# Performance work log

Measured on AMD Instinct MI355X. Metric: run time of the kernel, lower is better.

The kernel has to match this reference:

```python
import jax, jax.numpy as jnp
import numpy as np

E = 8        # num_experts
K = 2        # experts_per_token
D = 1024     # embed_dim
F = 4096     # expert intermediate (mlp_ratio * D)
FS = 2048    # shared-expert intermediate (n_shared_experts * D)
B, S = 2, 1024


def setup_inputs() -> dict:
    key = jax.random.key(0)
    ks = jax.random.split(key, 8)
    scale = jnp.float32(0.02)
    return {
        "x": jax.random.normal(ks[0], (B, S, D), jnp.float32),
        "gate_w": jax.random.normal(ks[1], (E, D), jnp.float32) * scale,
        "gate_k": jax.random.normal(ks[2], (E, D, F), jnp.float32) * scale,
        "up_k": jax.random.normal(ks[3], (E, D, F), jnp.float32) * scale,
        "down_k": jax.random.normal(ks[4], (E, F, D), jnp.float32) * scale,
        "sh_gate": jax.random.normal(ks[5], (D, FS), jnp.float32) * scale,
        "sh_up": jax.random.normal(ks[6], (D, FS), jnp.float32) * scale,
        "sh_down": jax.random.normal(ks[7], (FS, D), jnp.float32) * scale,
    }


def reference(x, gate_w, gate_k, up_k, down_k, sh_gate, sh_up, sh_down):
    b, s, d = x.shape
    xt = x.reshape(-1, d)                                   # [N, D] tokens

    # --- router gate: softmax over expert logits, then top-k ---
    logits = xt @ gate_w.T                                  # [N, E]
    scores = jax.nn.softmax(logits, axis=-1)
    topk_w, topk_i = jax.lax.top_k(scores, K)               # [N, K] each
    # norm_topk_prob = False -> use raw softmax top-k weights

    # per-token combine weights over experts: [N, E]
    combine = (jax.nn.one_hot(topk_i, E, dtype=xt.dtype) * topk_w[..., None]).sum(axis=1)

    # --- routed experts: SwiGLU MLP per expert (batched over E) ---
    g = jnp.einsum("nd,edf->enf", xt, gate_k)               # [E, N, F]
    u = jnp.einsum("nd,edf->enf", xt, up_k)                 # [E, N, F]
    a = jax.nn.silu(g) * u                                  # [E, N, F]
    eo = jnp.einsum("enf,efd->end", a, down_k)              # [E, N, D]
    y = jnp.einsum("end,ne->nd", eo, combine)               # [N, D]

    # --- shared expert (SwiGLU) on identity input ---
    shared = (jax.nn.silu(xt @ sh_gate) * (xt @ sh_up)) @ sh_down  # [N, D]

    return (y + shared).reshape(b, s, d)
```

## Files before the change

kernel.cpp:

```cpp
#include <hip/hip_runtime.h>
#include <hip/hip_bf16.h>

#define E_ 8
#define K_ 2
#define D_ 1024
#define F_ 4096
#define FS_ 2048
#define N_ 2048
#define ROWS_CAP 4352
#define TILE_CAP 40

typedef __bf16 bf16x8 __attribute__((ext_vector_type(8)));
typedef float f32x4 __attribute__((ext_vector_type(4)));

static __device__ __forceinline__ unsigned short f2bf(float f) {
  union { float f; unsigned int u; } v; v.f = f;
  unsigned int u = v.u;
  return (unsigned short)((u + 0x7FFF + ((u >> 16) & 1)) >> 16);
}

static __device__ __forceinline__ void gload16(const unsigned short* gp, unsigned short* lp) {
  __builtin_amdgcn_global_load_lds(
      (const __attribute__((address_space(1))) unsigned int*)gp,
      (__attribute__((address_space(3))) unsigned int*)lp, 16, 0, 0);
}

__global__ void init_k(int* counts) {
  if (threadIdx.x < E_) counts[threadIdx.x] = 0;
}

__global__ void router_k(const float* __restrict__ x, const float* __restrict__ gw,
                         unsigned short* __restrict__ xbf, float* __restrict__ topw,
                         int* __restrict__ topi, int* __restrict__ counts) {
  int wave = threadIdx.x >> 6, lane = threadIdx.x & 63;
  int n = blockIdx.x * 4 + wave;
  const float* xr = x + (size_t)n * D_;
  float v[16];
#pragma unroll
  for (int j = 0; j < 16; ++j) v[j] = xr[lane + 64 * j];
#pragma unroll
  for (int j = 0; j < 16; ++j) xbf[(size_t)n * D_ + lane + 64 * j] = f2bf(v[j]);
  float logit[E_];
  for (int e = 0; e < E_; ++e) {
    const float* g = gw + e * D_;
    float acc = 0.f;
#pragma unroll
    for (int j = 0; j < 16; ++j) acc += v[j] * g[lane + 64 * j];
#pragma unroll
    for (int off = 32; off > 0; off >>= 1) acc += __shfl_down(acc, off, 64);
    logit[e] = __shfl(acc, 0, 64);
  }
  if (lane == 0) {
    float m = logit[0];
    for (int e = 1; e < E_; ++e) m = fmaxf(m, logit[e]);
    float p[E_], s = 0.f;
    for (int e = 0; e < E_; ++e) { p[e] = expf(logit[e] - m); s += p[e]; }
    float inv = 1.f / s;
    for (int e = 0; e < E_; ++e) p[e] *= inv;
    int i0 = 0;
    for (int e = 1; e < E_; ++e) if (p[e] > p[i0]) i0 = e;
    int i1 = (i0 == 0) ? 1 : 0;
    for (int e = 0; e < E_; ++e) if (e != i0 && p[e] > p[i1]) i1 = e;
    topi[n * 2] = i0; topi[n * 2 + 1] = i1;
    topw[n * 2] = p[i0]; topw[n * 2 + 1] = p[i1];
    atomicAdd(&counts[i0], 1);
    atomicAdd(&counts[i1], 1);
  }
}

__global__ void scan_k(const int* __restrict__ counts, int* __restrict__ offs,
                       int* __restrict__ cursor, int* __restrict__ tile_e,
                       int* __restrict__ tile_m, int* __restrict__ ntiles) {
  if (threadIdx.x == 0) {
    int o = 0, idx = 0;
    for (int e = 0; e < E_; ++e) {
      offs[e] = o;
      int c = counts[e];
      int mt = (c + 127) >> 7;
      for (int m = 0; m < mt; ++m) {
        if (idx < TILE_CAP) { tile_e[idx] = e; tile_m[idx] = m; ++idx; }
      }
      o += c; cursor[e] = 0;
    }
    offs[E_] = o;
    ntiles[0] = idx;
  }
}

__global__ void fill_k(const int* __restrict__ topi, const int* __restrict__ offs,
                       int* __restrict__ cursor, int* __restrict__ rowlist,
                       int* __restrict__ slot_of) {
  int n = blockIdx.x * blockDim.x + threadIdx.x;
  if (n >= N_) return;
  for (int k = 0; k < K_; ++k) {
    int e = topi[n * 2 + k];
    int pos = offs[e] + atomicAdd(&cursor[e], 1);
    rowlist[pos] = n;
    slot_of[n * 2 + k] = pos;
  }
}

__global__ void transpose_cvt_k(const float* __restrict__ in, unsigned short* __restrict__ out,
                                int R, int C) {
  __shared__ float tile[64][65];
  int cb = blockIdx.x * 64, rb = blockIdx.y * 64;
  const float* ip = in + (size_t)blockIdx.z * R * C;
  unsigned short* op = out + (size_t)blockIdx.z * R * C;
  int t = threadIdx.x;
  int cx = t & 63, ry = t >> 6;
#pragma unroll
  for (int i = 0; i < 16; ++i)
    tile[ry + i * 4][cx] = ip[(size_t)(rb + ry + i * 4) * C + cb + cx];
  __syncthreads();
  int wx = t & 31, wy = t >> 5;
#pragma unroll
  for (int i = 0; i < 8; ++i) {
    int cl = wy + i * 8;
    unsigned int u = (unsigned int)f2bf(tile[2 * wx][cl]) |
                     ((unsigned int)f2bf(tile[2 * wx + 1][cl]) << 16);
    ((unsigned int*)(op + (size_t)(cb + cl) * R + rb))[wx] = u;
  }
}

__launch_bounds__(256, 3)
__global__ void gemm1_k(const unsigned short* __restrict__ Abase,
                        const int* __restrict__ rowlist,
                        const int* __restrict__ offs,
                        const int* __restrict__ tile_e, const int* __restrict__ tile_m,
                        const int* __restrict__ ntiles, int Mfixed,
                        const unsigned short* __restrict__ Bg_base,
                        const unsigned short* __restrict__ Bu_base,
                        int Ncols, int Kdim,
                        unsigned short* __restrict__ Out) {
  int e, mbase, Me, slotbase;
  if (tile_e) {
    if ((int)blockIdx.x >= ntiles[0]) return;
    e = tile_e[blockIdx.x]; mbase = tile_m[blockIdx.x] * 128;
    slotbase = offs[e]; Me = offs[e + 1] - slotbase;
  } else {
    e = 0; mbase = blockIdx.x * 128; slotbase = 0; Me = Mfixed;
  }
  int nbase = blockIdx.y * 64;
  const unsigned short* Bg = Bg_base + (size_t)e * Ncols * Kdim;
  const unsigned short* Bu = Bu_base + (size_t)e * Ncols * Kdim;

  __shared__ unsigned short As[128 * 32];
  __shared__ unsigned short Bgs[64 * 32];
  __shared__ unsigned short Bus[64 * 32];

  int t = threadIdx.x, lane = t & 63, wave = t >> 6;
  int wm = wave >> 1, wn = wave & 1;
  int chunk = lane & 3, rsub = lane >> 2;

  const unsigned short* aptr[2];
  unsigned int aoff[2];
#pragma unroll
  for (int i = 0; i < 2; ++i) {
    int r = wave * 32 + i * 16 + rsub;
    int grow = mbase + r;
    int src;
    if (rowlist) src = rowlist[slotbase + ((grow < Me) ? grow : 0)];
    else src = (grow < Me) ? grow : 0;
    aptr[i] = Abase + (size_t)src * Kdim + chunk * 8;
    aoff[i] = (unsigned)(wave * 32 + i * 16) * 32;
  }
  int bn = nbase + wave * 16 + rsub;
  const unsigned short* bgptr = Bg + (size_t)bn * Kdim + chunk * 8;
  const unsigned short* buptr = Bu + (size_t)bn * Kdim + chunk * 8;
  unsigned int boff = (unsigned)(wave * 16) * 32;

  f32x4 accg[4][2], accu[4][2];
#pragma unroll
  for (int i = 0; i < 4; ++i)
#pragma unroll
    for (int j = 0; j < 2; ++j) {
      accg[i][j] = f32x4{0.f, 0.f, 0.f, 0.f};
      accu[i][j] = f32x4{0.f, 0.f, 0.f, 0.f};
    }

  int nk = Kdim >> 5;
  for (int kt = 0; kt < nk; ++kt) {
    gload16(aptr[0] + kt * 32, &As[aoff[0]]);
    gload16(aptr[1] + kt * 32, &As[aoff[1]]);
    gload16(bgptr + kt * 32, &Bgs[boff]);
    gload16(buptr + kt * 32, &Bus[boff]);
    __syncthreads();
    bf16x8 afr[4];
#pragma unroll
    for (int i = 0; i < 4; ++i)
      afr[i] = *(const bf16x8*)&As[(wm * 64 + i * 16 + (lane & 15)) * 32 + (lane >> 4) * 8];
#pragma unroll
    for (int j = 0; j < 2; ++j) {
      bf16x8 bg = *(const bf16x8*)&Bgs[(wn * 32 + j * 16 + (lane & 15)) * 32 + (lane >> 4) * 8];
      bf16x8 bu = *(const bf16x8*)&Bus[(wn * 32 + j * 16 + (lane & 15)) * 32 + (lane >> 4) * 8];
#pragma unroll
      for (int i = 0; i < 4; ++i) {
        accg[i][j] = __builtin_amdgcn_mfma_f32_16x16x32_bf16(afr[i], bg, accg[i][j], 0, 0, 0);
        accu[i][j] = __builtin_amdgcn_mfma_f32_16x16x32_bf16(afr[i], bu, accu[i][j], 0, 0, 0);
      }
    }
    __syncthreads();
  }
  int r0 = (lane >> 4) * 4, cn = lane & 15;
#pragma unroll
  for (int i = 0; i < 4; ++i) {
#pragma unroll
    for (int rr = 0; rr < 4; ++rr) {
      int grow = mbase + wm * 64 + i * 16 + r0 + rr;
      if (grow < Me) {
        size_t rbase = (size_t)(slotbase + grow) * Ncols + nbase;
#pragma unroll
        for (int j = 0; j < 2; ++j) {
          float g = accg[i][j][rr], u = accu[i][j][rr];
          float a = (g / (1.f + __expf(-g))) * u;
          Out[rbase + wn * 32 + j * 16 + cn] = f2bf(a);
        }
      }
    }
  }
}

__launch_bounds__(256, 3)
__global__ void gemm2_k(const unsigned short* __restrict__ Abase,
                        const int* __restrict__ offs,
                        const int* __restrict__ tile_e, const int* __restrict__ tile_m,
                        const int* __restrict__ ntiles, int Mfixed,
                        const unsigned short* __restrict__ Bt_base,
                        int Ncols, int Kdim, int kchunk,
                        float* __restrict__ Out) {
  int e, mbase, Me, slotbase;
  if (tile_e) {
    if ((int)blockIdx.x >= ntiles[0]) return;
    e = tile_e[blockIdx.x]; mbase = tile_m[blockIdx.x] * 128;
    slotbase = offs[e]; Me = offs[e + 1] - slotbase;
  } else {
    e = 0; mbase = blockIdx.x * 128; slotbase = 0; Me = Mfixed;
  }
  int nbase = blockIdx.y * 128;
  int koff = blockIdx.z * kchunk;
  const unsigned short* Bt = Bt_base + (size_t)e * Ncols * Kdim;

  __shared__ unsigned short As[128 * 32];
  __shared__ unsigned short Bs[128 * 32];

  int t = threadIdx.x, lane = t & 63, wave = t >> 6;
  int wm = wave >> 1, wn = wave & 1;
  int chunk = lane & 3, rsub = lane >> 2;

  const unsigned short* aptr[2];
  const unsigned short* bptr[2];
  unsigned int loff[2];
#pragma unroll
  for (int i = 0; i < 2; ++i) {
    int r = wave * 32 + i * 16 + rsub;
    int grow = mbase + r;
    int arow = slotbase + ((grow < Me) ? grow : 0);
    aptr[i] = Abase + (size_t)arow * Kdim + koff + chunk * 8;
    bptr[i] = Bt + (size_t)(nbase + r) * Kdim + koff + chunk * 8;
    loff[i] = (unsigned)(wave * 32 + i * 16) * 32;
  }

  f32x4 acc[4][4];
#pragma unroll
  for (int i = 0; i < 4; ++i)
#pragma unroll
    for (int j = 0; j < 4; ++j) acc[i][j] = f32x4{0.f, 0.f, 0.f, 0.f};

  int nk = kchunk >> 5;
  for (int kt = 0; kt < nk; ++kt) {
    gload16(aptr[0] + kt * 32, &As[loff[0]]);
    gload16(aptr[1] + kt * 32, &As[loff[1]]);
    gload16(bptr[0] + kt * 32, &Bs[loff[0]]);
    gload16(bptr[1] + kt * 32, &Bs[loff[1]]);
    __syncthreads();
    bf16x8 afr[4];
#pragma unroll
    for (int i = 0; i < 4; ++i)
      afr[i] = *(const bf16x8*)&As[(wm * 64 + i * 16 + (lane & 15)) * 32 + (lane >> 4) * 8];
#pragma unroll
    for (int j = 0; j < 4; ++j) {
      bf16x8 bb = *(const bf16x8*)&Bs[(wn * 64 + j * 16 + (lane & 15)) * 32 + (lane >> 4) * 8];
#pragma unroll
      for (int i = 0; i < 4; ++i)
        acc[i][j] = __builtin_amdgcn_mfma_f32_16x16x32_bf16(afr[i], bb, acc[i][j], 0, 0, 0);
    }
    __syncthreads();
  }
  int r0 = (lane >> 4) * 4, cn = lane & 15;
#pragma unroll
  for (int i = 0; i < 4; ++i) {
#pragma unroll
    for (int rr = 0; rr < 4; ++rr) {
      int grow = mbase + wm * 64 + i * 16 + r0 + rr;
      if (grow < Me) {
        size_t rbase = (size_t)(slotbase + grow) * Ncols + nbase;
#pragma unroll
        for (int j = 0; j < 4; ++j)
          atomicAdd(&Out[rbase + wn * 64 + j * 16 + cn], acc[i][j][rr]);
      }
    }
  }
}

__launch_bounds__(256, 2)
__global__ void gemm1_old(const unsigned short* __restrict__ Abase,
                          const int* __restrict__ rowlist,
                          const int* __restrict__ offs, int Mfixed,
                          const float* __restrict__ Bg_base,
                          const float* __restrict__ Bu_base,
                          int Ncols, int Kdim,
                          unsigned short* __restrict__ Out) {
  int e = blockIdx.z;
  int Me, slotbase;
  if (offs) { slotbase = offs[e]; Me = offs[e + 1] - slotbase; }
  else      { slotbase = 0;       Me = Mfixed; }
  int mbase = blockIdx.x * 128;
  if (mbase >= Me) return;
  int nbase = blockIdx.y * 128;
  const float* Bg = Bg_base + (size_t)e * Kdim * Ncols;
  const float* Bu = Bu_base + (size_t)e * Kdim * Ncols;
  __shared__ unsigned short As[128][40];
  __shared__ unsigned short Bgs[128][40];
  __shared__ unsigned short Bus[128][40];
  int t = threadIdx.x, lane = t & 63, wave = t >> 6;
  int wm = wave >> 1, wn = wave & 1;
  f32x4 accg[4][4], accu[4][4];
#pragma unroll
  for (int i = 0; i < 4; ++i)
#pragma unroll
    for (int j = 0; j < 4; ++j) {
      accg[i][j] = f32x4{0.f, 0.f, 0.f, 0.f};
      accu[i][j] = f32x4{0.f, 0.f, 0.f, 0.f};
    }
  int ar = t >> 1, akh = t & 1;
  int arow = mbase + ar;
  int asrc = 0;
  if (arow < Me) asrc = rowlist ? rowlist[slotbase + arow] : arow;
  const unsigned short* aptr = Abase + (size_t)asrc * Kdim + akh * 16;
  int bfc = t & 127, bkh = t >> 7;
  const float* bgp = Bg + (size_t)(bkh * 16) * Ncols + nbase + bfc;
  const float* bup = Bu + (size_t)(bkh * 16) * Ncols + nbase + bfc;
  int nk = Kdim >> 5;
  for (int kt = 0; kt < nk; ++kt) {
    uint4 a0 = *(const uint4*)(aptr + kt * 32);
    uint4 a1 = *(const uint4*)(aptr + kt * 32 + 8);
    *(uint4*)&As[ar][akh * 16] = a0;
    *(uint4*)&As[ar][akh * 16 + 8] = a1;
    {
      const float* p0 = bgp + (size_t)kt * 32 * Ncols;
      float bv[16]; unsigned short h[16];
#pragma unroll
      for (int i = 0; i < 16; ++i) bv[i] = p0[(size_t)i * Ncols];
#pragma unroll
      for (int i = 0; i < 16; ++i) h[i] = f2bf(bv[i]);
      *(uint4*)&Bgs[bfc][bkh * 16] = *(uint4*)&h[0];
      *(uint4*)&Bgs[bfc][bkh * 16 + 8] = *(uint4*)&h[8];
    }
    {
      const float* p1 = bup + (size_t)kt * 32 * Ncols;
      float bv[16]; unsigned short h[16];
#pragma unroll
      for (int i = 0; i < 16; ++i) bv[i] = p1[(size_t)i * Ncols];
#pragma unroll
      for (int i = 0; i < 16; ++i) h[i] = f2bf(bv[i]);
      *(uint4*)&Bus[bfc][bkh * 16] = *(uint4*)&h[0];
      *(uint4*)&Bus[bfc][bkh * 16 + 8] = *(uint4*)&h[8];
    }
    __syncthreads();
    bf16x8 afr[4];
#pragma unroll
    for (int i = 0; i < 4; ++i)
      afr[i] = *(const bf16x8*)&As[wm * 64 + i * 16 + (lane & 15)][(lane >> 4) * 8];
#pragma unroll
    for (int j = 0; j < 4; ++j) {
      bf16x8 bg = *(const bf16x8*)&Bgs[wn * 64 + j * 16 + (lane & 15)][(lane >> 4) * 8];
      bf16x8 bu = *(const bf16x8*)&Bus[wn * 64 + j * 16 + (lane & 15)][(lane >> 4) * 8];
#pragma unroll
      for (int i = 0; i < 4; ++i) {
        accg[i][j] = __builtin_amdgcn_mfma_f32_16x16x32_bf16(afr[i], bg, accg[i][j], 0, 0, 0);
        accu[i][j] = __builtin_amdgcn_mfma_f32_16x16x32_bf16(afr[i], bu, accu[i][j], 0, 0, 0);
      }
    }
    __syncthreads();
  }
  int r0 = (lane >> 4) * 4, cn = lane & 15;
#pragma unroll
  for (int i = 0; i < 4; ++i) {
#pragma unroll
    for (int rr = 0; rr < 4; ++rr) {
      int grow = mbase + wm * 64 + i * 16 + r0 + rr;
      if (grow < Me) {
        size_t rbase = (size_t)(slotbase + grow) * Ncols + nbase;
#pragma unroll
        for (int j = 0; j < 4; ++j) {
          float g = accg[i][j][rr], u = accu[i][j][rr];
          float a = (g / (1.f + __expf(-g))) * u;
          Out[rbase + wn * 64 + j * 16 + cn] = f2bf(a);
        }
      }
    }
  }
}

__launch_bounds__(256, 2)
__global__ void gemm2_old(const unsigned short* __restrict__ Abase,
                          const int* __restrict__ offs, int Mfixed,
                          const float* __restrict__ B_base,
                          int Ncols, int Kdim,
                          float* __restrict__ Out) {
  int e = blockIdx.z;
  int Me, slotbase;
  if (offs) { slotbase = offs[e]; Me = offs[e + 1] - slotbase; }
  else      { slotbase = 0;       Me = Mfixed; }
  int mbase = blockIdx.x * 128;
  if (mbase >= Me) return;
  int nbase = blockIdx.y * 128;
  const float* B = B_base + (size_t)e * Kdim * Ncols;
  __shared__ unsigned short As[128][40];
  __shared__ unsigned short Bs[128][40];
  int t = threadIdx.x, lane = t & 63, wave = t >> 6;
  int wm = wave >> 1, wn = wave & 1;
  f32x4 acc[4][4];
#pragma unroll
  for (int i = 0; i < 4; ++i)
#pragma unroll
    for (int j = 0; j < 4; ++j) acc[i][j] = f32x4{0.f, 0.f, 0.f, 0.f};
  int ar = t >> 1, akh = t & 1;
  int arow = slotbase + ((mbase + ar < Me) ? (mbase + ar) : 0);
  const unsigned short* aptr = Abase + (size_t)arow * Kdim + akh * 16;
  int bfc = t & 127, bkh = t >> 7;
  const float* bp = B + (size_t)(bkh * 16) * Ncols + nbase + bfc;
  int nk = Kdim >> 5;
  for (int kt = 0; kt < nk; ++kt) {
    uint4 a0 = *(const uint4*)(aptr + kt * 32);
    uint4 a1 = *(const uint4*)(aptr + kt * 32 + 8);
    *(uint4*)&As[ar][akh * 16] = a0;
    *(uint4*)&As[ar][akh * 16 + 8] = a1;
    {
      const float* p0 = bp + (size_t)kt * 32 * Ncols;
      float bv[16]; unsigned short h[16];
#pragma unroll
      for (int i = 0; i < 16; ++i) bv[i] = p0[(size_t)i * Ncols];
#pragma unroll
      for (int i = 0; i < 16; ++i) h[i] = f2bf(bv[i]);
      *(uint4*)&Bs[bfc][bkh * 16] = *(uint4*)&h[0];
      *(uint4*)&Bs[bfc][bkh * 16 + 8] = *(uint4*)&h[8];
    }
    __syncthreads();
    bf16x8 afr[4];
#pragma unroll
    for (int i = 0; i < 4; ++i)
      afr[i] = *(const bf16x8*)&As[wm * 64 + i * 16 + (lane & 15)][(lane >> 4) * 8];
#pragma unroll
    for (int j = 0; j < 4; ++j) {
      bf16x8 bb = *(const bf16x8*)&Bs[wn * 64 + j * 16 + (lane & 15)][(lane >> 4) * 8];
#pragma unroll
      for (int i = 0; i < 4; ++i)
        acc[i][j] = __builtin_amdgcn_mfma_f32_16x16x32_bf16(afr[i], bb, acc[i][j], 0, 0, 0);
    }
    __syncthreads();
  }
  int r0 = (lane >> 4) * 4, cn = lane & 15;
#pragma unroll
  for (int i = 0; i < 4; ++i) {
#pragma unroll
    for (int rr = 0; rr < 4; ++rr) {
      int grow = mbase + wm * 64 + i * 16 + r0 + rr;
      if (grow < Me) {
        size_t rbase = (size_t)(slotbase + grow) * Ncols + nbase;
#pragma unroll
        for (int j = 0; j < 4; ++j)
          Out[rbase + wn * 64 + j * 16 + cn] = acc[i][j][rr];
      }
    }
  }
}

__global__ void combine_k(const float* __restrict__ eo, const float* __restrict__ sh,
                          const float* __restrict__ topw, const int* __restrict__ slot_of,
                          float* __restrict__ out) {
  int idx = blockIdx.x * blockDim.x + threadIdx.x;
  int n = idx >> 8;
  int d4 = idx & 255;
  float w0 = topw[n * 2], w1 = topw[n * 2 + 1];
  int s0 = slot_of[n * 2], s1 = slot_of[n * 2 + 1];
  float4 a = ((const float4*)(eo + (size_t)s0 * D_))[d4];
  float4 b = ((const float4*)(eo + (size_t)s1 * D_))[d4];
  float4 c = ((const float4*)(sh + (size_t)n * D_))[d4];
  float4 r;
  r.x = w0 * a.x + w1 * b.x + c.x;
  r.y = w0 * a.y + w1 * b.y + c.y;
  r.z = w0 * a.z + w1 * b.z + c.z;
  r.w = w0 * a.w + w1 * b.w + c.w;
  ((float4*)out)[idx] = r;
}

extern "C" void kernel_launch(void* const* d_in, const int* in_sizes, int n_in,
                              void* d_out, int out_size, void* d_ws, size_t ws_size,
                              hipStream_t stream) {
  const float* x  = (const float*)d_in[0];
  const float* gw = (const float*)d_in[1];
  const float* gk = (const float*)d_in[2];
  const float* uk = (const float*)d_in[3];
  const float* dk = (const float*)d_in[4];
  const float* sg = (const float*)d_in[5];
  const float* su = (const float*)d_in[6];
  const float* sd = (const float*)d_in[7];
  float* out = (float*)d_out;

  char* w = (char*)d_ws;
  size_t o = 0;
  auto take = [&](size_t bytes) -> void* {
    void* p = w + o;
    o += (bytes + 255) & ~(size_t)255;
    return p;
  };
  unsigned short* xbf    = (unsigned short*)take((size_t)N_ * D_ * 2);
  unsigned short* act    = (unsigned short*)take((size_t)ROWS_CAP * F_ * 2);
  unsigned short* act_sh = (unsigned short*)take((size_t)N_ * FS_ * 2);
  float* eo     = (float*)take((size_t)ROWS_CAP * D_ * 4);
  float* sh_out = (float*)take((size_t)N_ * D_ * 4);
  float* topw   = (float*)take((size_t)N_ * 2 * 4);
  int* topi     = (int*)take((size_t)N_ * 2 * 4);
  int* slot_of  = (int*)take((size_t)N_ * 2 * 4);
  int* rowlist  = (int*)take((size_t)ROWS_CAP * 4);
  int* counts   = (int*)take(E_ * 4);
  int* offs     = (int*)take((E_ + 1) * 4);
  int* cursor   = (int*)take(E_ * 4);
  int* tile_e   = (int*)take(TILE_CAP * 4);
  int* tile_m   = (int*)take(TILE_CAP * 4);
  int* ntiles   = (int*)take(4);
  unsigned short* gkt = (unsigned short*)take((size_t)E_ * D_ * F_ * 2);
  unsigned short* ukt = (unsigned short*)take((size_t)E_ * D_ * F_ * 2);
  unsigned short* dkt = (unsigned short*)take((size_t)E_ * D_ * F_ * 2);
  unsigned short* sgt = (unsigned short*)take((size_t)D_ * FS_ * 2);
  unsigned short* sut = (unsigned short*)take((size_t)D_ * FS_ * 2);
  unsigned short* sdt = (unsigned short*)take((size_t)D_ * FS_ * 2);
  bool full = (ws_size >= o);

  hipLaunchKernelGGL(init_k, dim3(1), dim3(64), 0, stream, counts);
  hipLaunchKernelGGL(router_k, dim3(N_ / 4), dim3(256), 0, stream,
                     x, gw, xbf, topw, topi, counts);
  hipLaunchKernelGGL(scan_k, dim3(1), dim3(32), 0, stream,
                     counts, offs, cursor, tile_e, tile_m, ntiles);
  hipLaunchKernelGGL(fill_k, dim3(N_ / 256), dim3(256), 0, stream,
                     topi, offs, cursor, rowlist, slot_of);

  if (full) {
    hipLaunchKernelGGL(transpose_cvt_k, dim3(F_ / 64, D_ / 64, E_), dim3(256), 0, stream,
                       gk, gkt, D_, F_);
    hipLaunchKernelGGL(transpose_cvt_k, dim3(F_ / 64, D_ / 64, E_), dim3(256), 0, stream,
                       uk, ukt, D_, F_);
    hipLaunchKernelGGL(transpose_cvt_k, dim3(D_ / 64, F_ / 64, E_), dim3(256), 0, stream,
                       dk, dkt, F_, D_);
    hipLaunchKernelGGL(transpose_cvt_k, dim3(FS_ / 64, D_ / 64, 1), dim3(256), 0, stream,
                       sg, sgt, D_, FS_);
    hipLaunchKernelGGL(transpose_cvt_k, dim3(FS_ / 64, D_ / 64, 1), dim3(256), 0, stream,
                       su, sut, D_, FS_);
    hipLaunchKernelGGL(transpose_cvt_k, dim3(D_ / 64, FS_ / 64, 1), dim3(256), 0, stream,
                       sd, sdt, FS_, D_);
    hipMemsetAsync(eo, 0, (size_t)ROWS_CAP * D_ * 4, stream);
    hipMemsetAsync(sh_out, 0, (size_t)N_ * D_ * 4, stream);
    hipLaunchKernelGGL(gemm1_k, dim3(TILE_CAP, F_ / 64), dim3(256), 0, stream,
                       xbf, rowlist, offs, tile_e, tile_m, ntiles, 0,
                       gkt, ukt, F_, D_, act);
    hipLaunchKernelGGL(gemm1_k, dim3(N_ / 128, FS_ / 64), dim3(256), 0, stream,
                       xbf, (const int*)nullptr, (const int*)nullptr,
                       (const int*)nullptr, (const int*)nullptr, (const int*)nullptr, N_,
                       sgt, sut, FS_, D_, act_sh);
    hipLaunchKernelGGL(gemm2_k, dim3(TILE_CAP, D_ / 128, 2), dim3(256), 0, stream,
                       act, offs, tile_e, tile_m, ntiles, 0,
                       dkt, D_, F_, F_ / 2, eo);
    hipLaunchKernelGGL(gemm2_k, dim3(N_ / 128, D_ / 128, 2), dim3(256), 0, stream,
                       act_sh, (const int*)nullptr, (const int*)nullptr,
                       (const int*)nullptr, (const int*)nullptr, N_,
                       sdt, D_, FS_, FS_ / 2, sh_out);
  } else {
    hipLaunchKernelGGL(gemm1_old, dim3(16, F_ / 128, E_), dim3(256), 0, stream,
                       xbf, rowlist, offs, 0, gk, uk, F_, D_, act);
    hipLaunchKernelGGL(gemm1_old, dim3(16, FS_ / 128, 1), dim3(256), 0, stream,
                       xbf, (const int*)nullptr, (const int*)nullptr, N_, sg, su, FS_, D_, act_sh);
    hipLaunchKernelGGL(gemm2_old, dim3(16, D_ / 128, E_), dim3(256), 0, stream,
                       act, offs, 0, dk, D_, F_, eo);
    hipLaunchKernelGGL(gemm2_old, dim3(16, D_ / 128, 1), dim3(256), 0, stream,
                       act_sh, (const int*)nullptr, N_, sd, D_, FS_, sh_out);
  }
  hipLaunchKernelGGL(combine_k, dim3((N_ * D_ / 4) / 256), dim3(256), 0, stream,
                     eo, sh_out, topw, slot_of, out);
}
```

Baseline: 779.8 us.

## Merge routing kernels, swizzle LDS, split-K partial buffers instead of atomics

Several changes land together. The init, scan and fill routing kernels become a single-block pack kernel that uses shared-memory atomics, and paired transposes are merged into one launch each. The GEMMs get an XOR swizzle on LDS chunk placement to cut bank conflicts, higher launch_bounds occupancy, and tile-grouped flattened block indexing meant to improve weight reuse in L2. gemm2 now uses 64-wide N tiles and writes its two split-K halves into separate partial buffers instead of doing atomicAdd, so the memsets are dropped and combine_k sums the partials, at the cost of extra memory traffic and workspace.

```diff
diff --git a/kernel.cpp b/kernel.cpp
--- a/kernel.cpp
+++ b/kernel.cpp
@@ -7,6 +7,7 @@
 #define F_ 4096
 #define FS_ 2048
 #define N_ 2048
+#define SLOTS 4096
 #define ROWS_CAP 4352
 #define TILE_CAP 40
 
@@ -25,13 +26,9 @@
       (__attribute__((address_space(3))) unsigned int*)lp, 16, 0, 0);
 }
 
-__global__ void init_k(int* counts) {
-  if (threadIdx.x < E_) counts[threadIdx.x] = 0;
-}
-
 __global__ void router_k(const float* __restrict__ x, const float* __restrict__ gw,
                          unsigned short* __restrict__ xbf, float* __restrict__ topw,
-                         int* __restrict__ topi, int* __restrict__ counts) {
+                         int* __restrict__ topi) {
   int wave = threadIdx.x >> 6, lane = threadIdx.x & 63;
   int n = blockIdx.x * 4 + wave;
   const float* xr = x + (size_t)n * D_;
@@ -63,49 +60,57 @@
     for (int e = 0; e < E_; ++e) if (e != i0 && p[e] > p[i1]) i1 = e;
     topi[n * 2] = i0; topi[n * 2 + 1] = i1;
     topw[n * 2] = p[i0]; topw[n * 2 + 1] = p[i1];
-    atomicAdd(&counts[i0], 1);
-    atomicAdd(&counts[i1], 1);
-  }
-}
-
-__global__ void scan_k(const int* __restrict__ counts, int* __restrict__ offs,
-                       int* __restrict__ cursor, int* __restrict__ tile_e,
-                       int* __restrict__ tile_m, int* __restrict__ ntiles) {
-  if (threadIdx.x == 0) {
+  }
+}
+
+__global__ void pack_k(const int* __restrict__ topi, int* __restrict__ offs,
+                       int* __restrict__ rowlist, int* __restrict__ slot_of,
+                       int* __restrict__ tile_e, int* __restrict__ tile_m,
+                       int* __restrict__ ntiles) {
+  __shared__ int cnt[E_], cur[E_], lo[E_ + 1];
+  int t = threadIdx.x;
+  if (t < E_) cnt[t] = 0;
+  __syncthreads();
+  for (int n = t; n < N_; n += 1024) {
+    atomicAdd(&cnt[topi[n * 2]], 1);
+    atomicAdd(&cnt[topi[n * 2 + 1]], 1);
+  }
+  __syncthreads();
+  if (t == 0) {
     int o = 0, idx = 0;
     for (int e = 0; e < E_; ++e) {
-      offs[e] = o;
-      int c = counts[e];
-      int mt = (c + 127) >> 7;
-      for (int m = 0; m < mt; ++m) {
-        if (idx < TILE_CAP) { tile_e[idx] = e; tile_m[idx] = m; ++idx; }
+      lo[e] = o; offs[e] = o;
+      int mt = (cnt[e] + 127) >> 7;
+      for (int m = 0; m < mt && idx < TILE_CAP; ++m) {
+        tile_e[idx] = e; tile_m[idx] = m; ++idx;
       }
-      o += c; cursor[e] = 0;
-    }
-    offs[E_] = o;
-    ntiles[0] = idx;
-  }
-}
-
-__global__ void fill_k(const int* __restrict__ topi, const int* __restrict__ offs,
-                       int* __restrict__ cursor, int* __restrict__ rowlist,
-                       int* __restrict__ slot_of) {
-  int n = blockIdx.x * blockDim.x + threadIdx.x;
-  if (n >= N_) return;
-  for (int k = 0; k < K_; ++k) {
-    int e = topi[n * 2 + k];
-    int pos = offs[e] + atomicAdd(&cursor[e], 1);
-    rowlist[pos] = n;
-    slot_of[n * 2 + k] = pos;
-  }
-}
-
-__global__ void transpose_cvt_k(const float* __restrict__ in, unsigned short* __restrict__ out,
-                                int R, int C) {
+      o += cnt[e];
+    }
+    lo[E_] = o; offs[E_] = o; ntiles[0] = idx;
+  }
+  if (t < E_) cur[t] = 0;
+  __syncthreads();
+  for (int n = t; n < N_; n += 1024) {
+    for (int k = 0; k < K_; ++k) {
+      int e = topi[n * 2 + k];
+      int pos = lo[e] + atomicAdd(&cur[e], 1);
+      rowlist[pos] = n;
+      slot_of[n * 2 + k] = pos;
+    }
+  }
+}
+
+__global__ void transpose_cvt_k(const float* __restrict__ in0, const float* __restrict__ in1,
+                                unsigned short* __restrict__ out0, unsigned short* __restrict__ out1,
+                                int R, int C, int zsplit) {
   __shared__ float tile[64][65];
+  int z = blockIdx.z;
+  const float* in = (z < zsplit) ? in0 : in1;
+  unsigned short* out = (z < zsplit) ? out0 : out1;
+  int zz = (z < zsplit) ? z : z - zsplit;
   int cb = blockIdx.x * 64, rb = blockIdx.y * 64;
-  const float* ip = in + (size_t)blockIdx.z * R * C;
-  unsigned short* op = out + (size_t)blockIdx.z * R * C;
+  const float* ip = in + (size_t)zz * R * C;
+  unsigned short* op = out + (size_t)zz * R * C;
   int t = threadIdx.x;
   int cx = t & 63, ry = t >> 6;
 #pragma unroll
@@ -122,7 +127,7 @@
   }
 }
 
-__launch_bounds__(256, 3)
+__launch_bounds__(256, 8)
 __global__ void gemm1_k(const unsigned short* __restrict__ Abase,
                         const int* __restrict__ rowlist,
                         const int* __restrict__ offs,
@@ -132,15 +137,19 @@
                         const unsigned short* __restrict__ Bu_base,
                         int Ncols, int Kdim,
                         unsigned short* __restrict__ Out) {
-  int e, mbase, Me, slotbase;
+  int e, mbase, Me, slotbase, ytile;
   if (tile_e) {
-    if ((int)blockIdx.x >= ntiles[0]) return;
-    e = tile_e[blockIdx.x]; mbase = tile_m[blockIdx.x] * 128;
+    int flat = blockIdx.x, c = flat & 7, t2 = flat >> 3;
+    ytile = c + 8 * (t2 & 7);
+    int xtile = t2 >> 3;
+    if (xtile >= ntiles[0]) return;
+    e = tile_e[xtile]; mbase = tile_m[xtile] * 128;
     slotbase = offs[e]; Me = offs[e + 1] - slotbase;
   } else {
     e = 0; mbase = blockIdx.x * 128; slotbase = 0; Me = Mfixed;
-  }
-  int nbase = blockIdx.y * 64;
+    ytile = blockIdx.y;
+  }
+  int nbase = ytile * 64;
   const unsigned short* Bg = Bg_base + (size_t)e * Ncols * Kdim;
   const unsigned short* Bu = Bu_base + (size_t)e * Ncols * Kdim;
 
@@ -150,7 +159,9 @@
 
   int t = threadIdx.x, lane = t & 63, wave = t >> 6;
   int wm = wave >> 1, wn = wave & 1;
-  int chunk = lane & 3, rsub = lane >> 2;
+  int rsub = lane >> 2;
+  int sw = (lane & 3) ^ (rsub & 3);
+  int fc = ((lane >> 4) ^ (lane & 3)) * 8;
 
   const unsigned short* aptr[2];
   unsigned int aoff[2];
@@ -161,12 +172,12 @@
     int src;
     if (rowlist) src = rowlist[slotbase + ((grow < Me) ? grow : 0)];
     else src = (grow < Me) ? grow : 0;
-    aptr[i] = Abase + (size_t)src * Kdim + chunk * 8;
+    aptr[i] = Abase + (size_t)src * Kdim + sw * 8;
     aoff[i] = (unsigned)(wave * 32 + i * 16) * 32;
   }
   int bn = nbase + wave * 16 + rsub;
-  const unsigned short* bgptr = Bg + (size_t)bn * Kdim + chunk * 8;
-  const unsigned short* buptr = Bu + (size_t)bn * Kdim + chunk * 8;
+  const unsigned short* bgptr = Bg + (size_t)bn * Kdim + sw * 8;
+  const unsigned short* buptr = Bu + (size_t)bn * Kdim + sw * 8;
   unsigned int boff = (unsigned)(wave * 16) * 32;
 
   f32x4 accg[4][2], accu[4][2];
@@ -188,11 +199,11 @@
     bf16x8 afr[4];
 #pragma unroll
     for (int i = 0; i < 4; ++i)
-      afr[i] = *(const bf16x8*)&As[(wm * 64 + i * 16 + (lane & 15)) * 32 + (lane >> 4) * 8];
+      afr[i] = *(const bf16x8*)&As[(wm * 64 + i * 16 + (lane & 15)) * 32 + fc];
 #pragma unroll
     for (int j = 0; j < 2; ++j) {
-      bf16x8 bg = *(const bf16x8*)&Bgs[(wn * 32 + j * 16 + (lane & 15)) * 32 + (lane >> 4) * 8];
-      bf16x8 bu = *(const bf16x8*)&Bus[(wn * 32 + j * 16 + (lane & 15)) * 32 + (lane >> 4) * 8];
+      bf16x8 bg = *(const bf16x8*)&Bgs[(wn * 32 + j * 16 + (lane & 15)) * 32 + fc];
+      bf16x8 bu = *(const bf16x8*)&Bus[(wn * 32 + j * 16 + (lane & 15)) * 32 + fc];
 #pragma unroll
       for (int i = 0; i < 4; ++i) {
         accg[i][j] = __builtin_amdgcn_mfma_f32_16x16x32_bf16(afr[i], bg, accg[i][j], 0, 0, 0);
@@ -220,66 +231,74 @@
   }
 }
 
-__launch_bounds__(256, 3)
+__launch_bounds__(256, 8)
 __global__ void gemm2_k(const unsigned short* __restrict__ Abase,
                         const int* __restrict__ offs,
                         const int* __restrict__ tile_e, const int* __restrict__ tile_m,
                         const int* __restrict__ ntiles, int Mfixed,
                         const unsigned short* __restrict__ Bt_base,
                         int Ncols, int Kdim, int kchunk,
-                        float* __restrict__ Out) {
-  int e, mbase, Me, slotbase;
+                        float* __restrict__ Out, size_t pstride) {
+  int e, mbase, Me, slotbase, ytile, ks;
   if (tile_e) {
-    if ((int)blockIdx.x >= ntiles[0]) return;
-    e = tile_e[blockIdx.x]; mbase = tile_m[blockIdx.x] * 128;
+    int flat = blockIdx.x, c = flat & 7, t2 = flat >> 3;
+    ytile = c + 8 * (t2 & 1);
+    int xtile = t2 >> 1;
+    if (xtile >= ntiles[0]) return;
+    e = tile_e[xtile]; mbase = tile_m[xtile] * 128;
     slotbase = offs[e]; Me = offs[e + 1] - slotbase;
+    ks = blockIdx.y;
   } else {
     e = 0; mbase = blockIdx.x * 128; slotbase = 0; Me = Mfixed;
-  }
-  int nbase = blockIdx.y * 128;
-  int koff = blockIdx.z * kchunk;
+    ytile = blockIdx.y; ks = blockIdx.z;
+  }
+  int nbase = ytile * 64;
+  int koff = ks * kchunk;
+  float* Outp = Out + (size_t)ks * pstride;
   const unsigned short* Bt = Bt_base + (size_t)e * Ncols * Kdim;
 
   __shared__ unsigned short As[128 * 32];
-  __shared__ unsigned short Bs[128 * 32];
+  __shared__ unsigned short Bs[64 * 32];
 
   int t = threadIdx.x, lane = t & 63, wave = t >> 6;
   int wm = wave >> 1, wn = wave & 1;
-  int chunk = lane & 3, rsub = lane >> 2;
+  int rsub = lane >> 2;
+  int sw = (lane & 3) ^ (rsub & 3);
+  int fc = ((lane >> 4) ^ (lane & 3)) * 8;
 
   const unsigned short* aptr[2];
-  const unsigned short* bptr[2];
-  unsigned int loff[2];
+  unsigned int aoff[2];
 #pragma unroll
   for (int i = 0; i < 2; ++i) {
     int r = wave * 32 + i * 16 + rsub;
     int grow = mbase + r;
     int arow = slotbase + ((grow < Me) ? grow : 0);
-    aptr[i] = Abase + (size_t)arow * Kdim + koff + chunk * 8;
-    bptr[i] = Bt + (size_t)(nbase + r) * Kdim + koff + chunk * 8;
-    loff[i] = (unsigned)(wave * 32 + i * 16) * 32;
-  }
-
-  f32x4 acc[4][4];
+    aptr[i] = Abase + (size_t)arow * Kdim + koff + sw * 8;
+    aoff[i] = (unsigned)(wave * 32 + i * 16) * 32;
+  }
+  int bn = nbase + wave * 16 + rsub;
+  const unsigned short* bptr = Bt + (size_t)bn * Kdim + koff + sw * 8;
+  unsigned int boff = (unsigned)(wave * 16) * 32;
+
+  f32x4 acc[4][2];
 #pragma unroll
   for (int i = 0; i < 4; ++i)
 #pragma unroll
-    for (int j = 0; j < 4; ++j) acc[i][j] = f32x4{0.f, 0.f, 0.f, 0.f};
+    for (int j = 0; j < 2; ++j) acc[i][j] = f32x4{0.f, 0.f, 0.f, 0.f};
 
   int nk = kchunk >> 5;
   for (int kt = 0; kt < nk; ++kt) {
-    gload16(aptr[0] + kt * 32, &As[loff[0]]);
-    gload16(aptr[1] + kt * 32, &As[loff[1]]);
-    gload16(bptr[0] + kt * 32, &Bs[loff[0]]);
-    gload16(bptr[1] + kt * 32, &Bs[loff[1]]);
+    gload16(aptr[0] + kt * 32, &As[aoff[0]]);
+    gload16(aptr[1] + kt * 32, &As[aoff[1]]);
+    gload16(bptr + kt * 32, &Bs[boff]);
     __syncthreads();
     bf16x8 afr[4];
 #pragma unroll
     for (int i = 0; i < 4; ++i)
-      afr[i] = *(const bf16x8*)&As[(wm * 64 + i * 16 + (lane & 15)) * 32 + (lane >> 4) * 8];
-#pragma unroll
-    for (int j = 0; j < 4; ++j) {
-      bf16x8 bb = *(const bf16x8*)&Bs[(wn * 64 + j * 16 + (lane & 15)) * 32 + (lane >> 4) * 8];
+      afr[i] = *(const bf16x8*)&As[(wm * 64 + i * 16 + (lane & 15)) * 32 + fc];
+#pragma unroll
+    for (int j = 0; j < 2; ++j) {
+      bf16x8 bb = *(const bf16x8*)&Bs[(wn * 32 + j * 16 + (lane & 15)) * 32 + fc];
 #pragma unroll
       for (int i = 0; i < 4; ++i)
         acc[i][j] = __builtin_amdgcn_mfma_f32_16x16x32_bf16(afr[i], bb, acc[i][j], 0, 0, 0);
@@ -295,8 +314,8 @@
       if (grow < Me) {
         size_t rbase = (size_t)(slotbase + grow) * Ncols + nbase;
 #pragma unroll
-        for (int j = 0; j < 4; ++j)
-          atomicAdd(&Out[rbase + wn * 64 + j * 16 + cn], acc[i][j][rr]);
+        for (int j = 0; j < 2; ++j)
+          Outp[rbase + wn * 32 + j * 16 + cn] = acc[i][j][rr];
       }
     }
   }
@@ -480,18 +499,20 @@
                           const float* __restrict__ topw, const int* __restrict__ slot_of,
                           float* __restrict__ out) {
   int idx = blockIdx.x * blockDim.x + threadIdx.x;
-  int n = idx >> 8;
-  int d4 = idx & 255;
+  int n = idx >> 8, d4 = idx & 255;
   float w0 = topw[n * 2], w1 = topw[n * 2 + 1];
   int s0 = slot_of[n * 2], s1 = slot_of[n * 2 + 1];
-  float4 a = ((const float4*)(eo + (size_t)s0 * D_))[d4];
-  float4 b = ((const float4*)(eo + (size_t)s1 * D_))[d4];
-  float4 c = ((const float4*)(sh + (size_t)n * D_))[d4];
+  const float4* e0 = (const float4*)eo;
+  const float4* e1 = (const float4*)(eo + (size_t)SLOTS * D_);
+  const float4* h0 = (const float4*)sh;
+  const float4* h1 = (const float4*)(sh + (size_t)N_ * D_);
+  size_t r0i = (size_t)s0 * 256 + d4, r1i = (size_t)s1 * 256 + d4, ni = (size_t)n * 256 + d4;
+  float4 a = e0[r0i], a1 = e1[r0i], b = e0[r1i], b1 = e1[r1i], c = h0[ni], c1 = h1[ni];
   float4 r;
-  r.x = w0 * a.x + w1 * b.x + c.x;
-  r.y = w0 * a.y + w1 * b.y + c.y;
-  r.z = w0 * a.z + w1 * b.z + c.z;
-  r.w = w0 * a.w + w1 * b.w + c.w;
+  r.x = w0 * (a.x + a1.x) + w1 * (b.x + b1.x) + c.x + c1.x;
+  r.y = w0 * (a.y + a1.y) + w1 * (b.y + b1.y) + c.y + c1.y;
+  r.z = w0 * (a.z + a1.z) + w1 * (b.z + b1.z) + c.z + c1.z;
+  r.w = w0 * (a.w + a1.w) + w1 * (b.w + b1.w) + c.w + c1.w;
   ((float4*)out)[idx] = r;
 }
 
@@ -516,17 +537,15 @@
     return p;
   };
   unsigned short* xbf    = (unsigned short*)take((size_t)N_ * D_ * 2);
-  unsigned short* act    = (unsigned short*)take((size_t)ROWS_CAP * F_ * 2);
+  unsigned short* act    = (unsigned short*)take((size_t)SLOTS * F_ * 2);
   unsigned short* act_sh = (unsigned short*)take((size_t)N_ * FS_ * 2);
-  float* eo     = (float*)take((size_t)ROWS_CAP * D_ * 4);
-  float* sh_out = (float*)take((size_t)N_ * D_ * 4);
+  float* eo     = (float*)take((size_t)2 * SLOTS * D_ * 4);
+  float* sh_out = (float*)take((size_t)2 * N_ * D_ * 4);
   float* topw   = (float*)take((size_t)N_ * 2 * 4);
   int* topi     = (int*)take((size_t)N_ * 2 * 4);
   int* slot_of  = (int*)take((size_t)N_ * 2 * 4);
   int* rowlist  = (int*)take((size_t)ROWS_CAP * 4);
-  int* counts   = (int*)take(E_ * 4);
   int* offs     = (int*)take((E_ + 1) * 4);
-  int* cursor   = (int*)take(E_ * 4);
   int* tile_e   = (int*)take(TILE_CAP * 4);
   int* tile_m   = (int*)take(TILE_CAP * 4);
   int* ntiles   = (int*)take(4);
@@ -538,44 +557,37 @@
   unsigned short* sdt = (unsigned short*)take((size_t)D_ * FS_ * 2);
   bool full = (ws_size >= o);
 
-  hipLaunchKernelGGL(init_k, dim3(1), dim3(64), 0, stream, counts);
   hipLaunchKernelGGL(router_k, dim3(N_ / 4), dim3(256), 0, stream,
-                     x, gw, xbf, topw, topi, counts);
-  hipLaunchKernelGGL(scan_k, dim3(1), dim3(32), 0, stream,
-                     counts, offs, cursor, tile_e, tile_m, ntiles);
-  hipLaunchKernelGGL(fill_k, dim3(N_ / 256), dim3(256), 0, stream,
-                     topi, offs, cursor, rowlist, slot_of);
+                     x, gw, xbf, topw, topi);
+  hipLaunchKernelGGL(pack_k, dim3(1), dim3(1024), 0, stream,
+                     topi, offs, rowlist, slot_of, tile_e, tile_m, ntiles);
 
   if (full) {
-    hipLaunchKernelGGL(transpose_cvt_k, dim3(F_ / 64, D_ / 64, E_), dim3(256), 0, stream,
-                       gk, gkt, D_, F_);
-    hipLaunchKernelGGL(transpose_cvt_k, dim3(F_ / 64, D_ / 64, E_), dim3(256), 0, stream,
-                       uk, ukt, D_, F_);
+    hipLaunchKernelGGL(transpose_cvt_k, dim3(F_ / 64, D_ / 64, 2 * E_), dim3(256), 0, stream,
+                       gk, uk, gkt, ukt, D_, F_, E_);
     hipLaunchKernelGGL(transpose_cvt_k, dim3(D_ / 64, F_ / 64, E_), dim3(256), 0, stream,
-                       dk, dkt, F_, D_);
-    hipLaunchKernelGGL(transpose_cvt_k, dim3(FS_ / 64, D_ / 64, 1), dim3(256), 0, stream,
-                       sg, sgt, D_, FS_);
-    hipLaunchKernelGGL(transpose_cvt_k, dim3(FS_ / 64, D_ / 64, 1), dim3(256), 0, stream,
-                       su, sut, D_, FS_);
+                       dk, dk, dkt, dkt, F_, D_, E_);
+    hipLaunchKernelGGL(transpose_cvt_k, dim3(FS_ / 64, D_ / 64, 2), dim3(256), 0, stream,
+                       sg, su, sgt, sut, D_, FS_, 1);
     hipLaunchKernelGGL(transpose_cvt_k, dim3(D_ / 64, FS_ / 64, 1), dim3(256), 0, stream,
-                       sd, sdt, FS_, D_);
-    hipMemsetAsync(eo, 0, (size_t)ROWS_CAP * D_ * 4, stream);
-    hipMemsetAsync(sh_out, 0, (size_t)N_ * D_ * 4, stream);
-    hipLaunchKernelGGL(gemm1_k, dim3(TILE_CAP, F_ / 64), dim3(256), 0, stream,
+                       sd, sd, sdt, sdt, FS_, D_, 1);
+    hipLaunchKernelGGL(gemm1_k, dim3(TILE_CAP * (F_ / 64)), dim3(256), 0, stream,
                        xbf, rowlist, offs, tile_e, tile_m, ntiles, 0,
                        gkt, ukt, F_, D_, act);
     hipLaunchKernelGGL(gemm1_k, dim3(N_ / 128, FS_ / 64), dim3(256), 0, stream,
                        xbf, (const int*)nullptr, (const int*)nullptr,
                        (const int*)nullptr, (const int*)nullptr, (const int*)nullptr, N_,
                        sgt, sut, FS_, D_, act_sh);
-    hipLaunchKernelGGL(gemm2_k, dim3(TILE_CAP, D_ / 128, 2), dim3(256), 0, stream,
+    hipLaunchKernelGGL(gemm2_k, dim3(TILE_CAP * (D_ / 64), 2), dim3(256), 0, stream,
                        act, offs, tile_e, tile_m, ntiles, 0,
-                       dkt, D_, F_, F_ / 2, eo);
-    hipLaunchKernelGGL(gemm2_k, dim3(N_ / 128, D_ / 128, 2), dim3(256), 0, stream,
+                       dkt, D_, F_, F_ / 2, eo, (size_t)SLOTS * D_);
+    hipLaunchKernelGGL(gemm2_k, dim3(N_ / 128, D_ / 64, 2), dim3(256), 0, stream,
                        act_sh, (const int*)nullptr, (const int*)nullptr,
                        (const int*)nullptr, (const int*)nullptr, N_,
-                       sdt, D_, FS_, FS_ / 2, sh_out);
+                       sdt, D_, FS_, FS_ / 2, sh_out, (size_t)N_ * D_);
   } else {
+    hipMemsetAsync(eo + (size_t)SLOTS * D_, 0, (size_t)SLOTS * D_ * 4, stream);
+    hipMemsetAsync(sh_out + (size_t)N_ * D_, 0, (size_t)N_ * D_ * 4, stream);
     hipLaunchKernelGGL(gemm1_old, dim3(16, F_ / 128, E_), dim3(256), 0, stream,
                        xbf, rowlist, offs, 0, gk, uk, F_, D_, act);
     hipLaunchKernelGGL(gemm1_old, dim3(16, FS_ / 128, 1), dim3(256), 0, stream,
```

New measurement: 1.859 ms. 2.38x slower.
